# Kernel tuning notes

Measured on AMD Instinct MI355X. Metric: run time of the kernel, lower is better.

The kernel has to match this reference:

```python
import jax, jax.numpy as jnp
import numpy as np

B, S, H, E = 64, 1024, 256, 256

def setup_inputs() -> dict:
    key = jax.random.key(0)
    k = jax.random.split(key, 6)
    scale = 1.0 / np.sqrt(H)
    return {
        "data_alpha": jax.random.normal(k[0], (B, S, H), jnp.float32),
        "data_beta": jax.random.normal(k[1], (B, S, H), jnp.float32),
        "data_embed": jax.random.normal(k[2], (B, S, E), jnp.float32),
        "data_mask": jnp.ones((B, S), jnp.float32),
        "Wb": jax.random.normal(k[3], (E, H), jnp.float32) * scale,
        "bb": jnp.zeros((E,), jnp.float32),
        "Wa": jax.random.normal(k[4], (H,), jnp.float32) * scale,
        "ba": jnp.zeros((1,), jnp.float32),
    }

def reference(data_alpha, data_beta, data_embed, data_mask, Wb, bb, Wa, ba):
    # beta gates: tanh(Linear(H->E))  [B,S,E]
    beta_w = jnp.tanh(jnp.einsum('bsh,eh->bse', data_beta, Wb) + bb)
    # alpha logits: Linear(H->1)  [B,S]
    corr = jnp.einsum('bsh,h->bs', data_alpha, Wa) + ba
    attn = jnp.exp(corr)[:, None, :]                       # [B,1,S]
    seq = data_alpha.shape[1]
    flag = jnp.triu(jnp.ones((seq, seq), data_alpha.dtype))[None]  # j >= i
    ef = flag * data_mask[:, None, :]                      # [B,S,S]
    num = attn * ef                                        # [B,S,S]
    acc = jnp.sum(num, axis=-1, keepdims=True) + 1e-10     # [B,S,1]
    alpha = num / acc                                      # [B,S,S]
    ew = beta_w * data_embed                               # [B,S,E]
    return jnp.einsum('bij,bje->bie', alpha, ew)           # [B,S,E]
```

## Files before the change

### kernel.cpp

```cpp
#include <hip/hip_runtime.h>
#include <hip/hip_bf16.h>

#define B_ 64
#define S_ 1024
#define H_ 256
#define E_ 256

#define EG_ 16
#define LDSB_ST 264
#define CH_ 128
#define NCH_ 8

typedef __attribute__((ext_vector_type(8))) __bf16 bf16x8;
typedef __attribute__((ext_vector_type(4))) __bf16 bf16x4;
typedef __attribute__((ext_vector_type(4))) float f32x4;

__global__ __launch_bounds__(256) void k0_prep(
        const float* __restrict__ alpha, const float* __restrict__ mask,
        const float* __restrict__ Wa,    const float* __restrict__ ba,
        const float* __restrict__ Wb,    const float* __restrict__ beta,
        __bf16* __restrict__ WbBf,       __bf16* __restrict__ betaBf,
        float* __restrict__ w) {
    const int tid = threadIdx.x, blk = blockIdx.x;
    if (blk >= 512) {
        const int base = (blk - 512) * 256 + tid;
        #pragma unroll 4
        for (int i = 0; i < 32; ++i) {
            const int idx = base + i * 131072;
            float4 v = ((const float4*)beta)[idx];
            bf16x4 bv;
            bv[0]=(__bf16)v.x; bv[1]=(__bf16)v.y; bv[2]=(__bf16)v.z; bv[3]=(__bf16)v.w;
            ((bf16x4*)betaBf)[idx] = bv;
        }
        return;
    }
    if (blk < 64) {
        int i = blk * 256 + tid;
        float4 v = ((const float4*)Wb)[i];
        bf16x4 bv;
        bv[0]=(__bf16)v.x; bv[1]=(__bf16)v.y; bv[2]=(__bf16)v.z; bv[3]=(__bf16)v.w;
        ((bf16x4*)WbBf)[i] = bv;
    }
    const int wv = tid >> 6, lane = tid & 63;
    const int rsub = lane >> 4, pcl = lane & 15;
    const float4* Wa4 = (const float4*)Wa;
    float4 wa0 = Wa4[pcl], wa1 = Wa4[pcl + 16],
           wa2 = Wa4[pcl + 32], wa3 = Wa4[pcl + 48];
    const float ba0 = ba[0];
    #pragma unroll 2
    for (int ps = 0; ps < 8; ++ps) {
        const int m = blk * 128 + ps * 16 + wv * 4 + rsub;
        const float4* ap = (const float4*)(alpha + (size_t)m * H_);
        float4 x0 = ap[pcl], x1 = ap[pcl + 16], x2 = ap[pcl + 32], x3 = ap[pcl + 48];
        float p = x0.x*wa0.x + x0.y*wa0.y + x0.z*wa0.z + x0.w*wa0.w
                + x1.x*wa1.x + x1.y*wa1.y + x1.z*wa1.z + x1.w*wa1.w
                + x2.x*wa2.x + x2.y*wa2.y + x2.z*wa2.z + x2.w*wa2.w
                + x3.x*wa3.x + x3.y*wa3.y + x3.z*wa3.z + x3.w*wa3.w;
        p += __shfl_xor(p, 1, 64);
        p += __shfl_xor(p, 2, 64);
        p += __shfl_xor(p, 4, 64);
        p += __shfl_xor(p, 8, 64);
        if (pcl == 0) w[m] = __expf(p + ba0) * mask[m];
    }
}

__global__ __launch_bounds__(512, 4) void k2_bf(
        const __bf16* __restrict__ betaBf, const float* __restrict__ embed,
        const __bf16* __restrict__ WbBf,   const float* __restrict__ bb,
        const float* __restrict__ w,       float* __restrict__ t) {
    __shared__ __bf16 ldsB[EG_ * LDSB_ST];
    __shared__ float wsLds[S_];
    __shared__ float ivLds[S_];
    __shared__ float red[2][8 * EG_];
    __shared__ float run[2][EG_];
    __shared__ float wsum[4];

    const int tid = threadIdx.x;
    const int wv = tid >> 6, lane = tid & 63;
    const int l15 = lane & 15, q = lane >> 4;
    const int blk = blockIdx.x;
    const int b  = blk & 63;
    const int eg = blk >> 6;

    {
        const int e = tid >> 5, ks = (tid & 31) * 8;
        *(bf16x8*)(ldsB + e * LDSB_ST + ks) =
            *(const bf16x8*)(WbBf + (size_t)(eg * EG_ + e) * H_ + ks);
    }
    if (tid < 256)
        *(float4*)(wsLds + tid * 4) = *(const float4*)(w + b * S_ + tid * 4);
    if (tid < 2 * EG_) run[tid >> 4][tid & 15] = 0.f;
    __syncthreads();

    {
        float w0 = 0, w1 = 0, w2 = 0, w3 = 0, tot = 0, suf = 0;
        const int sl = tid & 63, sw = tid >> 6;
        if (tid < 256) {
            w0 = wsLds[tid * 4];     w1 = wsLds[tid * 4 + 1];
            w2 = wsLds[tid * 4 + 2]; w3 = wsLds[tid * 4 + 3];
            tot = w0 + w1 + w2 + w3;
            suf = tot;
            #pragma unroll
            for (int off = 1; off < 64; off <<= 1) {
                float o = __shfl_down(suf, off, 64);
                if (sl + off < 64) suf += o;
            }
            if (sl == 0) wsum[sw] = suf;
        }
        __syncthreads();
        if (tid < 256) {
            float waveOff = 0.f;
            for (int j = sw + 1; j < 4; ++j) waveOff += wsum[j];
            float after = (suf - tot) + waveOff;
            float s3 = w3 + after, s2 = w2 + s3, s1 = w1 + s2, s0 = w0 + s1;
            ivLds[tid * 4]     = 1.f / (s0 + 1e-10f);
            ivLds[tid * 4 + 1] = 1.f / (s1 + 1e-10f);
            ivLds[tid * 4 + 2] = 1.f / (s2 + 1e-10f);
            ivLds[tid * 4 + 3] = 1.f / (s3 + 1e-10f);
        }
        __syncthreads();
    }

    const float bb0 = bb[eg * EG_ + l15];
    const __bf16* Abase = betaBf + ((size_t)b * S_ + wv * 16 + l15) * H_ + q * 8;
    const size_t ebase = ((size_t)b * S_ + wv * 16 + q * 4) * E_ + eg * EG_;
    const float* E0 = embed + ebase + l15;
    float* T0 = t + ebase + l15;

    bf16x8 nA[8];
    float eCur[4];
    {
        const size_t coff = (size_t)(NCH_ - 1) * CH_ * H_;
        #pragma unroll
        for (int kc = 0; kc < 8; ++kc)
            nA[kc] = *(const bf16x8*)(Abase + coff + (size_t)kc * 32);
        const size_t peoff = (size_t)(NCH_ - 1) * CH_ * E_;
        #pragma unroll
        for (int r = 0; r < 4; ++r)
            eCur[r] = E0[peoff + (size_t)r * E_];
    }

    #pragma unroll
    for (int si = 0; si < 8; ++si) {
        const int c = 7 - si;
        const int rb = si & 1;
        const size_t eoff = (size_t)c * CH_ * E_;

        bf16x8 curA[8];
        #pragma unroll
        for (int kc = 0; kc < 8; ++kc) curA[kc] = nA[kc];
        float eUse[4];
        #pragma unroll
        for (int r = 0; r < 4; ++r) eUse[r] = eCur[r];

        if (c > 0) {
            const size_t poff = (size_t)(c - 1) * CH_ * H_;
            #pragma unroll
            for (int kc = 0; kc < 8; ++kc)
                nA[kc] = *(const bf16x8*)(Abase + poff + (size_t)kc * 32);
            const size_t peoff = (size_t)(c - 1) * CH_ * E_;
            #pragma unroll
            for (int r = 0; r < 4; ++r)
                eCur[r] = E0[peoff + (size_t)r * E_];
        }

        f32x4 acc0 = {0.f, 0.f, 0.f, 0.f};
        #pragma unroll
        for (int kc = 0; kc < 8; ++kc) {
            bf16x8 bf0 = *(const bf16x8*)(ldsB + l15 * LDSB_ST + kc * 32 + q * 8);
            acc0 = __builtin_amdgcn_mfma_f32_16x16x32_bf16(curA[kc], bf0, acc0, 0, 0, 0);
        }

        float wmr[4], iv[4];
        #pragma unroll
        for (int r = 0; r < 4; ++r) {
            wmr[r] = wsLds[c * CH_ + wv * 16 + q * 4 + r];
            iv[r]  = ivLds[c * CH_ + wv * 16 + q * 4 + r];
        }
        float sv0[4];
        {
            float tv[4];
            #pragma unroll
            for (int r = 0; r < 4; ++r) {
                float x = acc0[r] + bb0;
                x = fminf(fmaxf(x, -15.f), 15.f);
                float ex = __expf(2.f * x);
                tv[r] = wmr[r] * ((ex - 1.f) / (ex + 1.f)) * eUse[r];
            }
            float s3 = tv[3], s2 = tv[2] + s3, s1 = tv[1] + s2, s0 = tv[0] + s1;
            float g = s0;
            float g1 = __shfl_down(g, 16, 64);
            float g2 = __shfl_down(g, 32, 64);
            float g3 = __shfl_down(g, 48, 64);
            float addG = (q < 3 ? g1 : 0.f) + (q < 2 ? g2 : 0.f) + (q < 1 ? g3 : 0.f);
            if (q == 0) red[rb][wv * EG_ + l15] = g + addG;
            sv0[0] = s0 + addG; sv0[1] = s1 + addG;
            sv0[2] = s2 + addG; sv0[3] = s3 + addG;
        }

        asm volatile("s_waitcnt lgkmcnt(0)" ::: "memory");
        __builtin_amdgcn_s_barrier();
        __builtin_amdgcn_sched_barrier(0);

        float nr0;
        {
            const float rn = run[rb][l15];
            float later = rn, tot = 0.f;
            #pragma unroll
            for (int w2 = 0; w2 < 8; ++w2) {
                float v = red[rb][w2 * EG_ + l15];
                tot += v;
                if (w2 > wv) later += v;
            }
            nr0 = rn + tot;
            #pragma unroll
            for (int r = 0; r < 4; ++r)
                T0[eoff + (size_t)r * E_] = (sv0[r] + later) * iv[r];
        }
        if (wv == 0 && q == 0)
            run[rb ^ 1][l15] = nr0;
    }
}

extern "C" void kernel_launch(void* const* d_in, const int* in_sizes, int n_in,
                              void* d_out, int out_size, void* d_ws, size_t ws_size,
                              hipStream_t stream) {
    const float* alpha = (const float*)d_in[0];
    const float* beta  = (const float*)d_in[1];
    const float* embed = (const float*)d_in[2];
    const float* mask  = (const float*)d_in[3];
    const float* Wb    = (const float*)d_in[4];
    const float* bbp   = (const float*)d_in[5];
    const float* Wa    = (const float*)d_in[6];
    const float* bap   = (const float*)d_in[7];

    char* ws = (char*)d_ws;
    float*  w      = (float*)ws;
    __bf16* WbBf   = (__bf16*)(ws + (256 << 10));
    __bf16* betaBf = (__bf16*)(ws + (512 << 10));

    k0_prep<<<1024, 256, 0, stream>>>(alpha, mask, Wa, bap, Wb, beta,
                                      WbBf, betaBf, w);
    k2_bf<<<B_ * (E_ / EG_), 512, 0, stream>>>(betaBf, embed, WbBf, bbp, w,
                                               (float*)d_out);
}
```

Baseline: 281.4 us.

## Widen per-block E tile to 32 columns to reuse beta A-fragments across two MFMAs

Each block now covers 32 embedding columns instead of 16. Every loaded bf16 beta fragment feeds two MFMA tiles, which halves how often the large beta matrix is re-read from memory across the grid. The block-to-(batch, e-group) mapping is also remapped so that neighbouring blocks share Wb rows and different batches are spread out. In exchange there are half as many blocks, more registers per thread for the second accumulator and embed values, and a second scan/reduction path, so occupancy and latency hiding may drop.

```diff
diff --git a/kernel.cpp b/kernel.cpp
--- a/kernel.cpp
+++ b/kernel.cpp
@@ -6,7 +6,7 @@
 #define H_ 256
 #define E_ 256
 
-#define EG_ 16
+#define EG_ 32
 #define LDSB_ST 264
 #define CH_ 128
 #define NCH_ 8
@@ -79,17 +79,18 @@
     const int wv = tid >> 6, lane = tid & 63;
     const int l15 = lane & 15, q = lane >> 4;
     const int blk = blockIdx.x;
-    const int b  = blk & 63;
-    const int eg = blk >> 6;
+    const int b  = (blk & 7) * 8 + (blk >> 6);
+    const int eg = (blk >> 3) & 7;
 
     {
-        const int e = tid >> 5, ks = (tid & 31) * 8;
-        *(bf16x8*)(ldsB + e * LDSB_ST + ks) =
-            *(const bf16x8*)(WbBf + (size_t)(eg * EG_ + e) * H_ + ks);
+        const int e = tid >> 4, kq = (tid & 15) * 16;
+        const __bf16* src = WbBf + (size_t)(eg * EG_ + e) * H_ + kq;
+        *(bf16x8*)(ldsB + e * LDSB_ST + kq)     = *(const bf16x8*)(src);
+        *(bf16x8*)(ldsB + e * LDSB_ST + kq + 8) = *(const bf16x8*)(src + 8);
     }
     if (tid < 256)
         *(float4*)(wsLds + tid * 4) = *(const float4*)(w + b * S_ + tid * 4);
-    if (tid < 2 * EG_) run[tid >> 4][tid & 15] = 0.f;
+    if (tid < 64) run[tid >> 5][tid & 31] = 0.f;
     __syncthreads();
 
     {
@@ -122,13 +123,16 @@
     }
 
     const float bb0 = bb[eg * EG_ + l15];
+    const float bb1 = bb[eg * EG_ + 16 + l15];
     const __bf16* Abase = betaBf + ((size_t)b * S_ + wv * 16 + l15) * H_ + q * 8;
     const size_t ebase = ((size_t)b * S_ + wv * 16 + q * 4) * E_ + eg * EG_;
     const float* E0 = embed + ebase + l15;
+    const float* E1 = E0 + 16;
     float* T0 = t + ebase + l15;
+    float* T1 = T0 + 16;
 
     bf16x8 nA[8];
-    float eCur[4];
+    float eCur0[4], eCur1[4];
     {
         const size_t coff = (size_t)(NCH_ - 1) * CH_ * H_;
         #pragma unroll
@@ -136,8 +140,10 @@
             nA[kc] = *(const bf16x8*)(Abase + coff + (size_t)kc * 32);
         const size_t peoff = (size_t)(NCH_ - 1) * CH_ * E_;
         #pragma unroll
-        for (int r = 0; r < 4; ++r)
-            eCur[r] = E0[peoff + (size_t)r * E_];
+        for (int r = 0; r < 4; ++r) {
+            eCur0[r] = E0[peoff + (size_t)r * E_];
+            eCur1[r] = E1[peoff + (size_t)r * E_];
+        }
     }
 
     #pragma unroll
@@ -149,9 +155,9 @@
         bf16x8 curA[8];
         #pragma unroll
         for (int kc = 0; kc < 8; ++kc) curA[kc] = nA[kc];
-        float eUse[4];
-        #pragma unroll
-        for (int r = 0; r < 4; ++r) eUse[r] = eCur[r];
+        float eUse0[4], eUse1[4];
+        #pragma unroll
+        for (int r = 0; r < 4; ++r) { eUse0[r] = eCur0[r]; eUse1[r] = eCur1[r]; }
 
         if (c > 0) {
             const size_t poff = (size_t)(c - 1) * CH_ * H_;
@@ -160,15 +166,19 @@
                 nA[kc] = *(const bf16x8*)(Abase + poff + (size_t)kc * 32);
             const size_t peoff = (size_t)(c - 1) * CH_ * E_;
             #pragma unroll
-            for (int r = 0; r < 4; ++r)
-                eCur[r] = E0[peoff + (size_t)r * E_];
-        }
-
-        f32x4 acc0 = {0.f, 0.f, 0.f, 0.f};
+            for (int r = 0; r < 4; ++r) {
+                eCur0[r] = E0[peoff + (size_t)r * E_];
+                eCur1[r] = E1[peoff + (size_t)r * E_];
+            }
+        }
+
+        f32x4 acc0 = {0.f, 0.f, 0.f, 0.f}, acc1 = {0.f, 0.f, 0.f, 0.f};
         #pragma unroll
         for (int kc = 0; kc < 8; ++kc) {
             bf16x8 bf0 = *(const bf16x8*)(ldsB + l15 * LDSB_ST + kc * 32 + q * 8);
+            bf16x8 bf1 = *(const bf16x8*)(ldsB + (16 + l15) * LDSB_ST + kc * 32 + q * 8);
             acc0 = __builtin_amdgcn_mfma_f32_16x16x32_bf16(curA[kc], bf0, acc0, 0, 0, 0);
+            acc1 = __builtin_amdgcn_mfma_f32_16x16x32_bf16(curA[kc], bf1, acc1, 0, 0, 0);
         }
 
         float wmr[4], iv[4];
@@ -177,7 +187,7 @@
             wmr[r] = wsLds[c * CH_ + wv * 16 + q * 4 + r];
             iv[r]  = ivLds[c * CH_ + wv * 16 + q * 4 + r];
         }
-        float sv0[4];
+        float sv0[4], sv1[4];
         {
             float tv[4];
             #pragma unroll
@@ -185,7 +195,7 @@
                 float x = acc0[r] + bb0;
                 x = fminf(fmaxf(x, -15.f), 15.f);
                 float ex = __expf(2.f * x);
-                tv[r] = wmr[r] * ((ex - 1.f) / (ex + 1.f)) * eUse[r];
+                tv[r] = wmr[r] * ((ex - 1.f) / (ex + 1.f)) * eUse0[r];
             }
             float s3 = tv[3], s2 = tv[2] + s3, s1 = tv[1] + s2, s0 = tv[0] + s1;
             float g = s0;
@@ -197,12 +207,31 @@
             sv0[0] = s0 + addG; sv0[1] = s1 + addG;
             sv0[2] = s2 + addG; sv0[3] = s3 + addG;
         }
+        {
+            float tv[4];
+            #pragma unroll
+            for (int r = 0; r < 4; ++r) {
+                float x = acc1[r] + bb1;
+                x = fminf(fmaxf(x, -15.f), 15.f);
+                float ex = __expf(2.f * x);
+                tv[r] = wmr[r] * ((ex - 1.f) / (ex + 1.f)) * eUse1[r];
+            }
+            float s3 = tv[3], s2 = tv[2] + s3, s1 = tv[1] + s2, s0 = tv[0] + s1;
+            float g = s0;
+            float g1 = __shfl_down(g, 16, 64);
+            float g2 = __shfl_down(g, 32, 64);
+            float g3 = __shfl_down(g, 48, 64);
+            float addG = (q < 3 ? g1 : 0.f) + (q < 2 ? g2 : 0.f) + (q < 1 ? g3 : 0.f);
+            if (q == 0) red[rb][wv * EG_ + 16 + l15] = g + addG;
+            sv1[0] = s0 + addG; sv1[1] = s1 + addG;
+            sv1[2] = s2 + addG; sv1[3] = s3 + addG;
+        }
 
         asm volatile("s_waitcnt lgkmcnt(0)" ::: "memory");
         __builtin_amdgcn_s_barrier();
         __builtin_amdgcn_sched_barrier(0);
 
-        float nr0;
+        float nr0, nr1;
         {
             const float rn = run[rb][l15];
             float later = rn, tot = 0.f;
@@ -217,8 +246,24 @@
             for (int r = 0; r < 4; ++r)
                 T0[eoff + (size_t)r * E_] = (sv0[r] + later) * iv[r];
         }
-        if (wv == 0 && q == 0)
+        {
+            const float rn = run[rb][16 + l15];
+            float later = rn, tot = 0.f;
+            #pragma unroll
+            for (int w2 = 0; w2 < 8; ++w2) {
+                float v = red[rb][w2 * EG_ + 16 + l15];
+                tot += v;
+                if (w2 > wv) later += v;
+            }
+            nr1 = rn + tot;
+            #pragma unroll
+            for (int r = 0; r < 4; ++r)
+                T1[eoff + (size_t)r * E_] = (sv1[r] + later) * iv[r];
+        }
+        if (wv == 0 && q == 0) {
             run[rb ^ 1][l15] = nr0;
+            run[rb ^ 1][16 + l15] = nr1;
+        }
     }
 }
 
```

New measurement: 260.1 us. 7.6% less time.
